# Performance work log

Hardware: AMD Instinct MI355X
Metric: run time of the kernel (lower is better)

Reference implementation:

```python
import jax, jax.numpy as jnp
import numpy as np

N, DIN, DOUT, E, H, C1 = 100000, 1000, 20, 1600000, 8, 8
BN_EPS = 1e-5
NEG_SLOPE = 0.2


def setup_inputs() -> dict:
    key = jax.random.key(0)
    ks = jax.random.split(key, 12)
    s = 0.05
    return {
        "x": jax.random.normal(ks[0], (N, DIN), jnp.float32),
        "edge_index": jax.random.randint(ks[1], (2, E), 0, N, jnp.int32),
        "bn_gamma": jnp.ones((DIN,), jnp.float32),
        "bn_beta": jnp.zeros((DIN,), jnp.float32),
        "W1": jax.random.normal(ks[2], (DIN, H * C1), jnp.float32) * s,
        "a_src1": jax.random.normal(ks[3], (H, C1), jnp.float32) * s,
        "a_dst1": jax.random.normal(ks[4], (H, C1), jnp.float32) * s,
        "b1": jnp.zeros((H * C1,), jnp.float32),
        "W2": jax.random.normal(ks[5], (H * C1, H * DOUT), jnp.float32) * s,
        "a_src2": jax.random.normal(ks[6], (H, DOUT), jnp.float32) * s,
        "a_dst2": jax.random.normal(ks[7], (H, DOUT), jnp.float32) * s,
        "b2": jnp.zeros((DOUT,), jnp.float32),
    }


def _gat(x, src, dst, W, a_src, a_dst, bias, heads, out_ch, concat):
    n = x.shape[0]
    h = (x @ W).reshape(n, heads, out_ch)              # [N,H,C]
    al_s = jnp.sum(h * a_src, axis=-1)                 # [N,H]
    al_d = jnp.sum(h * a_dst, axis=-1)                 # [N,H]
    e = al_s[src] + al_d[dst]                          # [E,H]
    e = jnp.where(e >= 0, e, NEG_SLOPE * e)            # leaky_relu(0.2)
    # segment softmax over incoming edges of each dst node
    m = jax.ops.segment_max(e, dst, num_segments=n)
    m = jnp.where(jnp.isfinite(m), m, 0.0)
    ex = jnp.exp(e - m[dst])
    denom = jax.ops.segment_sum(ex, dst, num_segments=n)
    alpha = ex / (denom[dst] + 1e-16)                  # [E,H]
    msg = h[src] * alpha[:, :, None]                   # [E,H,C]
    out = jax.ops.segment_sum(msg, dst, num_segments=n)  # [N,H,C]
    out = out.reshape(n, heads * out_ch) if concat else out.mean(axis=1)
    return out + bias


def reference(x, edge_index, bn_gamma, bn_beta, W1, a_src1, a_dst1, b1, W2, a_src2, a_dst2, b2):
    # BatchNorm1d (training-mode batch statistics, biased variance)
    mu = x.mean(axis=0)
    var = x.var(axis=0)
    xn = (x - mu) * jax.lax.rsqrt(var + BN_EPS) * bn_gamma + bn_beta
    # add self loops (PyG GATConv default add_self_loops=True)
    loops = jnp.arange(N, dtype=edge_index.dtype)
    src = jnp.concatenate([edge_index[0], loops])
    dst = jnp.concatenate([edge_index[1], loops])
    h = _gat(xn, src, dst, W1, a_src1, a_dst1, b1, H, C1, True)
    h = jax.nn.elu(h)
    out = _gat(h, src, dst, W2, a_src2, a_dst2, b2, H, DOUT, False)
    return jax.nn.log_softmax(out, axis=1)
```

## Files before the change

kernel.cpp:

```cpp
#include <hip/hip_runtime.h>
#include <math.h>

#define N_NODES 100000
#define D_IN    1000
#define D_OUT   20
#define N_HEAD  8
#define C_ONE   8
#define SCAN_CHUNK 512
#define NCH ((N_NODES + SCAN_CHUNK - 1) / SCAN_CHUNK)

#define BM 128
#define BN 64
#define BK 64
#define KPAD 1024
#define KTILES 16
#define G1_BLOCKS ((N_NODES + BM - 1) / BM)
#define BN_BLOCKS 500
#define NPART BN_BLOCKS
#define PREP_BLOCKS 297

static constexpr float kBnEps = 1e-5f;
static constexpr float kSlope = 0.2f;

typedef __attribute__((ext_vector_type(8))) short short8;
typedef __attribute__((ext_vector_type(4))) short sh4;
typedef __attribute__((ext_vector_type(4))) float f32x4;

__device__ __forceinline__ unsigned short f2bf(float f) {
    unsigned u = __float_as_uint(f);
    unsigned r = (u + 0x7fffu + ((u >> 16) & 1u)) >> 16;
    return (unsigned short)r;
}
__device__ __forceinline__ float bf2f(short s) {
    unsigned u = ((unsigned)(unsigned short)s) << 16;
    return __uint_as_float(u);
}

__global__ __launch_bounds__(256) void k_phase1(const float* __restrict__ x,
                                                float* __restrict__ ps,
                                                const int* __restrict__ ei,
                                                int E, int TE,
                                                int* __restrict__ deg) {
    int b = blockIdx.x, tid = threadIdx.x;
    if (b < BN_BLOCKS) {
        int c4 = tid;
        if (c4 >= 250) return;
        int r0 = b * 200;
        float4 s = make_float4(0.f, 0.f, 0.f, 0.f);
        float4 q = make_float4(0.f, 0.f, 0.f, 0.f);
        const char* base = (const char*)x + (size_t)r0 * (D_IN * 4) + (size_t)c4 * 16;
        for (int i = 0; i < 200; i += 8) {
            float4 v[8];
            #pragma unroll
            for (int j = 0; j < 8; ++j)
                v[j] = *(const float4*)(base + (size_t)(i + j) * (D_IN * 4));
            #pragma unroll
            for (int j = 0; j < 8; ++j) {
                s.x += v[j].x; s.y += v[j].y; s.z += v[j].z; s.w += v[j].w;
                q.x += v[j].x * v[j].x; q.y += v[j].y * v[j].y;
                q.z += v[j].z * v[j].z; q.w += v[j].w * v[j].w;
            }
        }
        *(float4*)(ps + (size_t)b * 2000 + c4 * 4) = s;
        *(float4*)(ps + (size_t)b * 2000 + 1000 + c4 * 4) = q;
    } else {
        int eid = (b - BN_BLOCKS) * 256 + tid;
        if (eid >= TE) return;
        int dst = (eid < E) ? ei[E + eid] : (eid - E);
        atomicAdd(&deg[dst], 1);
    }
}

__global__ void k_reduce(const float* __restrict__ ps,
                         float* __restrict__ cs, float* __restrict__ cs2) {
    int cg = blockIdx.x & 3;
    int ch = blockIdx.x >> 2;
    int c = cg * 256 + threadIdx.x;
    if (c >= D_IN) return;
    int b0 = ch * (NPART / 10), b1 = b0 + (NPART / 10);
    float s = 0.f, s2 = 0.f;
    #pragma unroll 5
    for (int b = b0; b < b1; ++b) {
        s  += ps[(size_t)b * 2000 + c];
        s2 += ps[(size_t)b * 2000 + 1000 + c];
    }
    atomicAdd(&cs[c], s);
    atomicAdd(&cs2[c], s2);
}

__global__ void k_phase2(const int* __restrict__ deg, int* __restrict__ csum,
                         const float* __restrict__ W1, const float* __restrict__ W2,
                         const float* __restrict__ cs, const float* __restrict__ cs2,
                         const float* __restrict__ gamma, const float* __restrict__ beta,
                         short* __restrict__ W1t, short* __restrict__ W2t,
                         float* __restrict__ c1) {
    __shared__ int red[4];
    __shared__ float part[4][64];
    int b = blockIdx.x, tid = threadIdx.x;
    if (b < NCH) {
        int i0 = b * SCAN_CHUNK + tid * 2;
        int a = (i0 < N_NODES) ? deg[i0] : 0;
        int bb = (i0 + 1 < N_NODES) ? deg[i0 + 1] : 0;
        int t = a + bb;
        #pragma unroll
        for (int d = 1; d < 64; d <<= 1) t += __shfl_xor(t, d);
        if ((tid & 63) == 0) red[tid >> 6] = t;
        __syncthreads();
        if (tid == 0) csum[b] = red[0] + red[1] + red[2] + red[3];
        return;
    }
    int pb = b - NCH;
    if (pb < 256) {
        int idx = pb * 256 + tid;
        int n = idx >> 10, k = idx & (KPAD - 1);
        float v = 0.f;
        if (k < D_IN) {
            float mu  = cs[k]  * (1.f / N_NODES);
            float var = cs2[k] * (1.f / N_NODES) - mu * mu;
            float sc  = rsqrtf(var + kBnEps) * gamma[k];
            v = W1[k * 64 + n] * sc;
        }
        W1t[idx] = (short)f2bf(v);
    } else if (pb < 296) {
        int idx = (pb - 256) * 256 + tid;
        if (idx < 160 * 64) {
            int n = idx >> 6, k = idx & 63;
            W2t[idx] = (short)f2bf(W2[k * 160 + n]);
        }
    } else {
        int j  = tid & 63;
        int kc = tid >> 6;
        float acc = 0.f;
        for (int k = kc * 250; k < (kc + 1) * 250; ++k) {
            float mu  = cs[k]  * (1.f / N_NODES);
            float var = cs2[k] * (1.f / N_NODES) - mu * mu;
            float sc  = rsqrtf(var + kBnEps) * gamma[k];
            float sh  = beta[k] - mu * sc;
            acc += sh * W1[k * 64 + j];
        }
        part[kc][j] = acc;
        __syncthreads();
        if (kc == 0) c1[j] = part[0][j] + part[1][j] + part[2][j] + part[3][j];
    }
}

__global__ void k_scan_c(const int* __restrict__ deg, const int* __restrict__ csum,
                         int TE, int* __restrict__ row_start, int* __restrict__ cursor) {
    __shared__ int wsum1[4];
    __shared__ int wsum2[4];
    __shared__ int base_sh;
    int c = blockIdx.x, tid = threadIdx.x;
    int lane = tid & 63, w = tid >> 6;

    int pv = (tid < c) ? csum[tid] : 0;
    #pragma unroll
    for (int d = 1; d < 64; d <<= 1) pv += __shfl_xor(pv, d);
    if (lane == 0) wsum1[w] = pv;
    __syncthreads();
    if (tid == 0) base_sh = wsum1[0] + wsum1[1] + wsum1[2] + wsum1[3];

    int i0 = c * SCAN_CHUNK + tid * 2;
    int a = (i0 < N_NODES) ? deg[i0] : 0;
    int b = (i0 + 1 < N_NODES) ? deg[i0 + 1] : 0;
    int t = a + b;
    int incl = t;
    #pragma unroll
    for (int d = 1; d < 64; d <<= 1) {
        int v = __shfl_up(incl, d);
        if (lane >= d) incl += v;
    }
    if (lane == 63) wsum2[w] = incl;
    __syncthreads();
    int wbase = 0;
    for (int k = 0; k < w; ++k) wbase += wsum2[k];
    int ex = base_sh + wbase + incl - t;
    if (i0 < N_NODES)     { row_start[i0] = ex;         cursor[i0] = ex; }
    if (i0 + 1 < N_NODES) { row_start[i0 + 1] = ex + a; cursor[i0 + 1] = ex + a; }
    if (c == 0 && tid == 0) row_start[N_NODES] = TE;
}

__global__ __launch_bounds__(256) void k_phase4(const float* __restrict__ x,
                                                const short* __restrict__ W1t,
                                                const float* __restrict__ c1,
                                                const float* __restrict__ a_src1,
                                                const float* __restrict__ a_dst1,
                                                short* __restrict__ h1b,
                                                float* __restrict__ als,
                                                float* __restrict__ ald,
                                                const int* __restrict__ ei,
                                                int E, int TE,
                                                int* __restrict__ cursor,
                                                int* __restrict__ srcs) {
    __shared__ short lA[BM * BK];
    __shared__ short lB[BN * BK];

    int tid = threadIdx.x;
    if ((int)blockIdx.x >= G1_BLOCKS) {
        int eid = ((int)blockIdx.x - G1_BLOCKS) * 256 + tid;
        if (eid < TE) {
            int src, dst;
            if (eid < E) { src = ei[eid]; dst = ei[E + eid]; }
            else { src = eid - E; dst = src; }
            int pos = atomicAdd(&cursor[dst], 1);
            srcs[pos] = src;
        }
        return;
    }

    int lane = tid & 63;
    int wave = tid >> 6;
    int l15  = lane & 15, kq = lane >> 4;
    int row0 = blockIdx.x * BM;
    int wm0  = wave * 32;

    f32x4 zero4 = {0.f, 0.f, 0.f, 0.f};
    f32x4 acc[2][4];
    #pragma unroll
    for (int m = 0; m < 2; ++m)
        #pragma unroll
        for (int n = 0; n < 4; ++n) acc[m][n] = zero4;

    int ar = tid >> 4;
    int akf4 = tid & 15;

    for (int kt = 0; kt < KTILES; ++kt) {
        int k0 = kt * BK;
        bool kok = (k0 + akf4 * 4) < D_IN;
        #pragma unroll
        for (int p = 0; p < 8; ++p) {
            int r = ar + p * 16;
            int gr = row0 + r;
            float4 v = make_float4(0.f, 0.f, 0.f, 0.f);
            if (gr < N_NODES && kok)
                v = *(const float4*)(x + (size_t)gr * D_IN + k0 + akf4 * 4);
            unsigned lo = f2bf(v.x) | ((unsigned)f2bf(v.y) << 16);
            unsigned hi = f2bf(v.z) | ((unsigned)f2bf(v.w) << 16);
            int off = r * 128 + ((((akf4 >> 1) ^ (r & 7)) << 4) | ((akf4 & 1) << 3));
            *(uint2*)((char*)lA + off) = make_uint2(lo, hi);
        }
        #pragma unroll
        for (int c = tid; c < 512; c += 256) {
            int n = c >> 3, s = c & 7;
            short8 v = *(const short8*)((const char*)W1t + n * (KPAD * 2) + k0 * 2 + (s << 4));
            int off = n * 128 + ((s ^ (n & 7)) << 4);
            *(short8*)((char*)lB + off) = v;
        }
        __syncthreads();
        #pragma unroll
        for (int h = 0; h < 2; ++h) {
            short8 aF[2], bF[4];
            #pragma unroll
            for (int m = 0; m < 2; ++m) {
                int row = wm0 + m * 16 + l15;
                int off = row * 128 + (((((h << 2) + kq)) ^ (row & 7)) << 4);
                aF[m] = *(const short8*)((const char*)lA + off);
            }
            #pragma unroll
            for (int n = 0; n < 4; ++n) {
                int col = n * 16 + l15;
                int off = col * 128 + (((((h << 2) + kq)) ^ (col & 7)) << 4);
                bF[n] = *(const short8*)((const char*)lB + off);
            }
            #pragma unroll
            for (int m = 0; m < 2; ++m)
                #pragma unroll
                for (int n = 0; n < 4; ++n)
                    acc[m][n] = __builtin_amdgcn_mfma_f32_16x16x32_bf16(aF[m], bF[n], acc[m][n], 0, 0, 0);
        }
        __syncthreads();
    }

    float cv[4];
    #pragma unroll
    for (int n = 0; n < 4; ++n) cv[n] = c1[n * 16 + l15];
    #pragma unroll
    for (int m = 0; m < 2; ++m)
        #pragma unroll
        for (int q = 0; q < 4; ++q) {
            int rl = wm0 + m * 16 + (kq << 2) + q;
            #pragma unroll
            for (int n = 0; n < 4; ++n)
                lA[rl * 64 + n * 16 + l15] = (short)f2bf(acc[m][n][q] + cv[n]);
        }
    __syncthreads();
    #pragma unroll
    for (int idx = tid; idx < 1024; idx += 256) {
        int r = idx >> 3, s = idx & 7;
        int gr = row0 + r;
        if (gr < N_NODES)
            *(short8*)((char*)h1b + (size_t)gr * 128 + (s << 4)) =
                *(const short8*)((const char*)lA + r * 128 + (s << 4));
    }
    #pragma unroll
    for (int pair = tid; pair < 1024; pair += 256) {
        int r = pair >> 3, hd = pair & 7;
        int gr = row0 + r;
        if (gr >= N_NODES) continue;
        short8 v = *(const short8*)((const char*)lA + r * 128 + hd * 16);
        float s = 0.f, d = 0.f;
        #pragma unroll
        for (int c = 0; c < 8; ++c) {
            float f = bf2f(v[c]);
            s += f * a_src1[hd * 8 + c];
            d += f * a_dst1[hd * 8 + c];
        }
        als[gr * 8 + hd] = s;
        ald[gr * 8 + hd] = d;
    }
}

__global__ __launch_bounds__(512) void k_fused_l2(const int* __restrict__ row_start,
                                                  const int* __restrict__ srcs,
                                                  const float* __restrict__ als1,
                                                  const float* __restrict__ ald1,
                                                  const short* __restrict__ h1b,
                                                  const float* __restrict__ b1,
                                                  const short* __restrict__ W2t,
                                                  const float* __restrict__ a_src2,
                                                  const float* __restrict__ a_dst2,
                                                  short* __restrict__ h2b,
                                                  float* __restrict__ als2,
                                                  float* __restrict__ ald2) {
    __shared__ __align__(16) char smem[40960];
    short* lA  = (short*)smem;
    short* lB  = (short*)(smem + 16384);
    short* stg = (short*)smem;

    int tid  = threadIdx.x;
    int lane = tid & 63;
    int wave = tid >> 6;
    int l15  = lane & 15, kq = lane >> 4;
    int row0 = blockIdx.x * 128;
    int wm0  = wave * 16;

    for (int idx = tid; idx < 1280; idx += 512) {
        int n = idx >> 3, s = idx & 7;
        short8 v = *(const short8*)((const char*)W2t + n * 128 + (s << 4));
        int off = n * 128 + ((s ^ (n & 7)) << 4);
        *(short8*)((char*)lB + off) = v;
    }

    #pragma unroll
    for (int pp = 0; pp < 2; ++pp) {
        int pair = tid + pp * 512;
        int r = pair >> 3, hd = pair & 7;
        int dst = row0 + r;
        short8 o = {0, 0, 0, 0, 0, 0, 0, 0};
        if (dst < N_NODES) {
            int beg = row_start[dst], end = row_start[dst + 1];
            float ad = ald1[dst * 8 + hd];
            float sum = 0.f;
            float acc[C_ONE] = {};
            for (int e = beg; e < end; ++e) {
                int s = srcs[e];
                float v = als1[s * 8 + hd] + ad;
                v = v >= 0.f ? v : kSlope * v;
                float wgt = __expf(v);
                short8 hv = *(const short8*)((const char*)h1b + (size_t)s * 128 + hd * 16);
                sum += wgt;
                #pragma unroll
                for (int c = 0; c < C_ONE; ++c) acc[c] += wgt * bf2f(hv[c]);
            }
            float inv = 1.f / (sum + 1e-16f);
            #pragma unroll
            for (int c = 0; c < C_ONE; ++c) {
                float v = acc[c] * inv + b1[hd * 8 + c];
                v = v > 0.f ? v : __expf(v) - 1.f;
                o[c] = (short)f2bf(v);
            }
        }
        int off = r * 128 + ((hd ^ (r & 7)) << 4);
        *(short8*)((char*)lA + off) = o;
    }
    __syncthreads();

    f32x4 zero4 = {0.f, 0.f, 0.f, 0.f};
    f32x4 acc2[10];
    #pragma unroll
    for (int n = 0; n < 10; ++n) acc2[n] = zero4;

    #pragma unroll
    for (int hh = 0; hh < 2; ++hh) {
        short8 aF, bF[10];
        {
            int row = wm0 + l15;
            int off = row * 128 + ((((hh << 2) + kq) ^ (row & 7)) << 4);
            aF = *(const short8*)((const char*)lA + off);
        }
        #pragma unroll
        for (int n = 0; n < 10; ++n) {
            int col = n * 16 + l15;
            int off = col * 128 + ((((hh << 2) + kq) ^ (col & 7)) << 4);
            bF[n] = *(const short8*)((const char*)lB + off);
        }
        #pragma unroll
        for (int n = 0; n < 10; ++n)
            acc2[n] = __builtin_amdgcn_mfma_f32_16x16x32_bf16(aF, bF[n], acc2[n], 0, 0, 0);
    }
    __syncthreads();

    #pragma unroll
    for (int q = 0; q < 4; ++q) {
        int rl = wm0 + (kq << 2) + q;
        #pragma unroll
        for (int n = 0; n < 10; ++n)
            stg[rl * 160 + n * 16 + l15] = (short)f2bf(acc2[n][q]);
    }
    __syncthreads();

    for (int pair = tid; pair < 1024; pair += 512) {
        int r = pair >> 3, hd = pair & 7;
        int dst = row0 + r;
        if (dst >= N_NODES) continue;
        const char* hp = (const char*)stg + r * 320 + hd * 40;
        float s = 0.f, d = 0.f;
        #pragma unroll
        for (int p = 0; p < 5; ++p) {
            sh4 v = *(const sh4*)(hp + p * 8);
            #pragma unroll
            for (int j = 0; j < 4; ++j) {
                float f = bf2f(v[j]);
                s += f * a_src2[hd * 20 + p * 4 + j];
                d += f * a_dst2[hd * 20 + p * 4 + j];
            }
        }
        als2[dst * 8 + hd] = s;
        ald2[dst * 8 + hd] = d;
    }
    for (int idx = tid; idx < 2560; idx += 512) {
        int r = idx / 20, c8 = idx % 20;
        int gr = row0 + r;
        if (gr < N_NODES)
            *(short8*)((char*)h2b + (size_t)gr * 320 + (c8 << 4)) =
                *(const short8*)((const char*)stg + r * 320 + (c8 << 4));
    }
}

__global__ __launch_bounds__(256) void k_gather2(const int* __restrict__ row_start,
                                                 const int* __restrict__ srcs,
                                                 const float* __restrict__ als,
                                                 const float* __restrict__ ald,
                                                 const short* __restrict__ h2,
                                                 const float* __restrict__ b2,
                                                 float* __restrict__ out) {
    int idx = blockIdx.x * blockDim.x + threadIdx.x;
    if (idx >= N_NODES * 16) return;
    int dst  = idx >> 4;
    int sub  = idx & 15;
    int hd   = sub >> 1;
    int half = sub & 1;
    int beg0 = row_start[dst], end0 = row_start[dst + 1];
    int mid  = beg0 + ((end0 - beg0 + 1) >> 1);
    int beg  = half ? mid : beg0;
    int end  = half ? end0 : mid;
    float ad = ald[dst * 8 + hd];
    float sum = 0.f;
    float acc[D_OUT] = {};
    for (int e = beg; e < end; ++e) {
        int s = srcs[e];
        float v = als[s * 8 + hd] + ad;
        v = v >= 0.f ? v : kSlope * v;
        float wgt = __expf(v);
        const char* hp = (const char*)h2 + (size_t)s * 320 + hd * 40;
        sum += wgt;
        #pragma unroll
        for (int p = 0; p < 5; ++p) {
            sh4 t = *(const sh4*)(hp + p * 8);
            #pragma unroll
            for (int j = 0; j < 4; ++j) acc[p * 4 + j] += wgt * bf2f(t[j]);
        }
    }
    sum += __shfl_xor(sum, 1);
    float inv = 1.f / (sum + 1e-16f);
    #pragma unroll
    for (int c = 0; c < D_OUT; ++c) {
        float v = acc[c];
        v += __shfl_xor(v, 1);
        v *= inv;
        v += __shfl_xor(v, 2);
        v += __shfl_xor(v, 4);
        v += __shfl_xor(v, 8);
        acc[c] = v;
    }
    if (sub == 0) {
        float vals[D_OUT];
        float mx = -1e30f;
        #pragma unroll
        for (int c = 0; c < D_OUT; ++c) {
            vals[c] = 0.125f * acc[c] + b2[c];
            mx = fmaxf(mx, vals[c]);
        }
        float s = 0.f;
        #pragma unroll
        for (int c = 0; c < D_OUT; ++c) s += __expf(vals[c] - mx);
        float lse = mx + __logf(s);
        float* op = out + (size_t)dst * D_OUT;
        #pragma unroll
        for (int c = 0; c < D_OUT; ++c) op[c] = vals[c] - lse;
    }
}

extern "C" void kernel_launch(void* const* d_in, const int* in_sizes, int n_in,
                              void* d_out, int out_size, void* d_ws, size_t ws_size,
                              hipStream_t stream) {
    const float* x      = (const float*)d_in[0];
    const int*   ei     = (const int*)d_in[1];
    const float* gamma  = (const float*)d_in[2];
    const float* beta   = (const float*)d_in[3];
    const float* W1     = (const float*)d_in[4];
    const float* a_src1 = (const float*)d_in[5];
    const float* a_dst1 = (const float*)d_in[6];
    const float* b1     = (const float*)d_in[7];
    const float* W2     = (const float*)d_in[8];
    const float* a_src2 = (const float*)d_in[9];
    const float* a_dst2 = (const float*)d_in[10];
    const float* b2     = (const float*)d_in[11];
    float* out = (float*)d_out;
    (void)n_in; (void)out_size; (void)ws_size;

    const int E  = in_sizes[1] / 2;
    const int TE = E + N_NODES;

    char* wsb = (char*)d_ws;
    size_t off = 0;
    auto alloc = [&](size_t bytes) -> void* {
        void* p = wsb + off;
        off += (bytes + 255) & ~(size_t)255;
        return p;
    };
    float* cs    = (float*)alloc(D_IN * sizeof(float));
    float* cs2   = (float*)alloc(D_IN * sizeof(float));
    float* ps    = (float*)alloc((size_t)NPART * 2000 * sizeof(float));
    short* W1t   = (short*)alloc((size_t)64 * KPAD * sizeof(short));
    short* W2t   = (short*)alloc((size_t)160 * 64 * sizeof(short));
    float* c1    = (float*)alloc(64 * sizeof(float));
    short* h1b   = (short*)alloc((size_t)N_NODES * 64 * sizeof(short));
    short* h2b   = (short*)alloc((size_t)N_NODES * 160 * sizeof(short));
    float* als   = (float*)alloc((size_t)N_NODES * N_HEAD * sizeof(float));
    float* ald   = (float*)alloc((size_t)N_NODES * N_HEAD * sizeof(float));
    float* als2  = (float*)alloc((size_t)N_NODES * N_HEAD * sizeof(float));
    float* ald2  = (float*)alloc((size_t)N_NODES * N_HEAD * sizeof(float));
    int*   deg   = (int*)alloc((size_t)N_NODES * sizeof(int));
    int*   rs    = (int*)alloc((size_t)(N_NODES + 1) * sizeof(int));
    int*   cur   = (int*)alloc((size_t)N_NODES * sizeof(int));
    int*   csum  = (int*)alloc((size_t)NCH * sizeof(int));
    int*   srcs  = (int*)alloc((size_t)TE * sizeof(int));

    int egrid = (TE + 255) / 256;

    hipMemsetAsync(deg, 0, (size_t)N_NODES * sizeof(int), stream);
    hipMemsetAsync(cs, 0, 8192, stream);

    k_phase1<<<BN_BLOCKS + egrid, 256, 0, stream>>>(x, ps, ei, E, TE, deg);

    k_reduce<<<40, 256, 0, stream>>>(ps, cs, cs2);

    k_phase2<<<NCH + PREP_BLOCKS, 256, 0, stream>>>(deg, csum, W1, W2, cs, cs2,
                                                     gamma, beta, W1t, W2t, c1);

    k_scan_c<<<NCH, 256, 0, stream>>>(deg, csum, TE, rs, cur);

    k_phase4<<<G1_BLOCKS + egrid, 256, 0, stream>>>(x, W1t, c1, a_src1, a_dst1,
                                                     h1b, als, ald, ei, E, TE, cur, srcs);

    k_fused_l2<<<(N_NODES + 127) / 128, 512, 0, stream>>>(rs, srcs, als, ald, h1b, b1,
                                                           W2t, a_src2, a_dst2,
                                                           h2b, als2, ald2);

    k_gather2<<<(N_NODES * 16 + 255) / 256, 256, 0, stream>>>(rs, srcs, als2, ald2,
                                                               h2b, b2, out);
}
```

Measured before the change: 460.8 us.

## Reassociate layer-2 GAT: aggregate 64-wide features before applying W2

Layer 2 no longer projects every node to 160 features. Instead it stores the 64-wide ELU output. The attention logits come from precomputed folded vectors, W2·a_src2 and W2·a_dst2. The gather kernel builds per-head weighted sums of the 64-wide source features, sharing each head's weight across 8 lanes with shuffles. It then applies W2 once per destination node. This cuts per-edge gather bytes and removes the MFMA projection and the large h2 write. The cost is more per-edge FMAs (64 per lane), more registers, and a per-node matvec that reads W2t from global memory.

```diff
diff --git a/kernel.cpp b/kernel.cpp
--- a/kernel.cpp
+++ b/kernel.cpp
@@ -17,7 +17,7 @@
 #define G1_BLOCKS ((N_NODES + BM - 1) / BM)
 #define BN_BLOCKS 500
 #define NPART BN_BLOCKS
-#define PREP_BLOCKS 297
+#define PREP_BLOCKS 298
 
 static constexpr float kBnEps = 1e-5f;
 static constexpr float kSlope = 0.2f;
@@ -92,8 +92,10 @@
                          const float* __restrict__ W1, const float* __restrict__ W2,
                          const float* __restrict__ cs, const float* __restrict__ cs2,
                          const float* __restrict__ gamma, const float* __restrict__ beta,
+                         const float* __restrict__ a_src2, const float* __restrict__ a_dst2,
                          short* __restrict__ W1t, short* __restrict__ W2t,
-                         float* __restrict__ c1) {
+                         float* __restrict__ c1,
+                         float* __restrict__ wt_s, float* __restrict__ wt_d) {
     __shared__ int red[4];
     __shared__ float part[4][64];
     int b = blockIdx.x, tid = threadIdx.x;
@@ -127,7 +129,7 @@
             int n = idx >> 6, k = idx & 63;
             W2t[idx] = (short)f2bf(W2[k * 160 + n]);
         }
-    } else {
+    } else if (pb == 296) {
         int j  = tid & 63;
         int kc = tid >> 6;
         float acc = 0.f;
@@ -141,6 +143,21 @@
         part[kc][j] = acc;
         __syncthreads();
         if (kc == 0) c1[j] = part[0][j] + part[1][j] + part[2][j] + part[3][j];
+    } else {
+        #pragma unroll
+        for (int it = 0; it < 2; ++it) {
+            int idx = it * 256 + tid;
+            int h = idx >> 6, k = idx & 63;
+            float ss = 0.f, dd = 0.f;
+            #pragma unroll
+            for (int c = 0; c < 20; ++c) {
+                float w = W2[k * 160 + h * 20 + c];
+                ss += w * a_src2[h * 20 + c];
+                dd += w * a_dst2[h * 20 + c];
+            }
+            wt_s[h * 64 + k] = ss;
+            wt_d[h * 64 + k] = dd;
+        }
     }
 }
 
@@ -315,30 +332,19 @@
                                                   const float* __restrict__ ald1,
                                                   const short* __restrict__ h1b,
                                                   const float* __restrict__ b1,
-                                                  const short* __restrict__ W2t,
-                                                  const float* __restrict__ a_src2,
-                                                  const float* __restrict__ a_dst2,
-                                                  short* __restrict__ h2b,
+                                                  const float* __restrict__ wt_s,
+                                                  const float* __restrict__ wt_d,
+                                                  short* __restrict__ out1b,
                                                   float* __restrict__ als2,
                                                   float* __restrict__ ald2) {
-    __shared__ __align__(16) char smem[40960];
-    short* lA  = (short*)smem;
-    short* lB  = (short*)(smem + 16384);
-    short* stg = (short*)smem;
+    __shared__ short lA[128 * 64];
+    __shared__ float lWs[512];
+    __shared__ float lWd[512];
 
     int tid  = threadIdx.x;
-    int lane = tid & 63;
-    int wave = tid >> 6;
-    int l15  = lane & 15, kq = lane >> 4;
     int row0 = blockIdx.x * 128;
-    int wm0  = wave * 16;
-
-    for (int idx = tid; idx < 1280; idx += 512) {
-        int n = idx >> 3, s = idx & 7;
-        short8 v = *(const short8*)((const char*)W2t + n * 128 + (s << 4));
-        int off = n * 128 + ((s ^ (n & 7)) << 4);
-        *(short8*)((char*)lB + off) = v;
-    }
+
+    if (tid < 512) { lWs[tid] = wt_s[tid]; lWd[tid] = wt_d[tid]; }
 
     #pragma unroll
     for (int pp = 0; pp < 2; ++pp) {
@@ -374,65 +380,35 @@
     }
     __syncthreads();
 
-    f32x4 zero4 = {0.f, 0.f, 0.f, 0.f};
-    f32x4 acc2[10];
-    #pragma unroll
-    for (int n = 0; n < 10; ++n) acc2[n] = zero4;
-
-    #pragma unroll
-    for (int hh = 0; hh < 2; ++hh) {
-        short8 aF, bF[10];
-        {
-            int row = wm0 + l15;
-            int off = row * 128 + ((((hh << 2) + kq) ^ (row & 7)) << 4);
-            aF = *(const short8*)((const char*)lA + off);
-        }
-        #pragma unroll
-        for (int n = 0; n < 10; ++n) {
-            int col = n * 16 + l15;
-            int off = col * 128 + ((((hh << 2) + kq) ^ (col & 7)) << 4);
-            bF[n] = *(const short8*)((const char*)lB + off);
-        }
-        #pragma unroll
-        for (int n = 0; n < 10; ++n)
-            acc2[n] = __builtin_amdgcn_mfma_f32_16x16x32_bf16(aF, bF[n], acc2[n], 0, 0, 0);
-    }
-    __syncthreads();
-
-    #pragma unroll
-    for (int q = 0; q < 4; ++q) {
-        int rl = wm0 + (kq << 2) + q;
-        #pragma unroll
-        for (int n = 0; n < 10; ++n)
-            stg[rl * 160 + n * 16 + l15] = (short)f2bf(acc2[n][q]);
-    }
-    __syncthreads();
-
-    for (int pair = tid; pair < 1024; pair += 512) {
+    #pragma unroll
+    for (int pp = 0; pp < 2; ++pp) {
+        int idx = tid + pp * 512;
+        int r = idx >> 3, s = idx & 7;
+        int gr = row0 + r;
+        if (gr < N_NODES)
+            *(short8*)((char*)out1b + (size_t)gr * 128 + (s << 4)) =
+                *(const short8*)((const char*)lA + r * 128 + ((s ^ (r & 7)) << 4));
+    }
+
+    #pragma unroll
+    for (int pp = 0; pp < 2; ++pp) {
+        int pair = tid + pp * 512;
         int r = pair >> 3, hd = pair & 7;
         int dst = row0 + r;
         if (dst >= N_NODES) continue;
-        const char* hp = (const char*)stg + r * 320 + hd * 40;
         float s = 0.f, d = 0.f;
         #pragma unroll
-        for (int p = 0; p < 5; ++p) {
-            sh4 v = *(const sh4*)(hp + p * 8);
-            #pragma unroll
-            for (int j = 0; j < 4; ++j) {
-                float f = bf2f(v[j]);
-                s += f * a_src2[hd * 20 + p * 4 + j];
-                d += f * a_dst2[hd * 20 + p * 4 + j];
+        for (int ch = 0; ch < 8; ++ch) {
+            short8 v = *(const short8*)((const char*)lA + r * 128 + ((ch ^ (r & 7)) << 4));
+            #pragma unroll
+            for (int c = 0; c < 8; ++c) {
+                float f = bf2f(v[c]);
+                s += f * lWs[hd * 64 + ch * 8 + c];
+                d += f * lWd[hd * 64 + ch * 8 + c];
             }
         }
         als2[dst * 8 + hd] = s;
         ald2[dst * 8 + hd] = d;
-    }
-    for (int idx = tid; idx < 2560; idx += 512) {
-        int r = idx / 20, c8 = idx % 20;
-        int gr = row0 + r;
-        if (gr < N_NODES)
-            *(short8*)((char*)h2b + (size_t)gr * 320 + (c8 << 4)) =
-                *(const short8*)((const char*)stg + r * 320 + (c8 << 4));
     }
 }
 
@@ -440,60 +416,91 @@
                                                  const int* __restrict__ srcs,
                                                  const float* __restrict__ als,
                                                  const float* __restrict__ ald,
-                                                 const short* __restrict__ h2,
+                                                 const short* __restrict__ out1b,
+                                                 const short* __restrict__ W2t,
                                                  const float* __restrict__ b2,
                                                  float* __restrict__ out) {
-    int idx = blockIdx.x * blockDim.x + threadIdx.x;
-    if (idx >= N_NODES * 16) return;
-    int dst  = idx >> 4;
-    int sub  = idx & 15;
-    int hd   = sub >> 1;
-    int half = sub & 1;
-    int beg0 = row_start[dst], end0 = row_start[dst + 1];
-    int mid  = beg0 + ((end0 - beg0 + 1) >> 1);
-    int beg  = half ? mid : beg0;
-    int end  = half ? end0 : mid;
-    float ad = ald[dst * 8 + hd];
-    float sum = 0.f;
-    float acc[D_OUT] = {};
+    int tid = threadIdx.x;
+    int g = tid >> 3, j = tid & 7;
+    int dst = blockIdx.x * 32 + g;
+    if (dst >= N_NODES) return;
+
+    int beg = row_start[dst], end = row_start[dst + 1];
+    float adj = ald[dst * 8 + j];
+    float Agg[8][8] = {};
+    float mysum = 0.f;
+
     for (int e = beg; e < end; ++e) {
         int s = srcs[e];
-        float v = als[s * 8 + hd] + ad;
+        float v = als[s * 8 + j] + adj;
         v = v >= 0.f ? v : kSlope * v;
-        float wgt = __expf(v);
-        const char* hp = (const char*)h2 + (size_t)s * 320 + hd * 40;
-        sum += wgt;
-        #pragma unroll
-        for (int p = 0; p < 5; ++p) {
-            sh4 t = *(const sh4*)(hp + p * 8);
-            #pragma unroll
-            for (int j = 0; j < 4; ++j) acc[p * 4 + j] += wgt * bf2f(t[j]);
-        }
-    }
-    sum += __shfl_xor(sum, 1);
-    float inv = 1.f / (sum + 1e-16f);
+        float w = __expf(v);
+        mysum += w;
+        float a0 = w;
+        float a1 = __shfl_xor(a0, 1);
+        float a2 = __shfl_xor(a0, 2);
+        float a3 = __shfl_xor(a1, 2);
+        float a4 = __shfl_xor(a0, 4);
+        float a5 = __shfl_xor(a1, 4);
+        float a6 = __shfl_xor(a2, 4);
+        float a7 = __shfl_xor(a3, 4);
+        short8 hv = *(const short8*)((const char*)out1b + (size_t)s * 128 + j * 16);
+        float f[8];
+        #pragma unroll
+        for (int c = 0; c < 8; ++c) f[c] = bf2f(hv[c]);
+        #pragma unroll
+        for (int c = 0; c < 8; ++c) {
+            Agg[0][c] += a0 * f[c];
+            Agg[1][c] += a1 * f[c];
+            Agg[2][c] += a2 * f[c];
+            Agg[3][c] += a3 * f[c];
+            Agg[4][c] += a4 * f[c];
+            Agg[5][c] += a5 * f[c];
+            Agg[6][c] += a6 * f[c];
+            Agg[7][c] += a7 * f[c];
+        }
+    }
+
+    float s0 = mysum;
+    float s1 = __shfl_xor(s0, 1);
+    float s2 = __shfl_xor(s0, 2);
+    float s3 = __shfl_xor(s1, 2);
+    float s4 = __shfl_xor(s0, 4);
+    float s5 = __shfl_xor(s1, 4);
+    float s6 = __shfl_xor(s2, 4);
+    float s7 = __shfl_xor(s3, 4);
+    float iS[8];
+    iS[0] = 1.f / (s0 + 1e-16f); iS[1] = 1.f / (s1 + 1e-16f);
+    iS[2] = 1.f / (s2 + 1e-16f); iS[3] = 1.f / (s3 + 1e-16f);
+    iS[4] = 1.f / (s4 + 1e-16f); iS[5] = 1.f / (s5 + 1e-16f);
+    iS[6] = 1.f / (s6 + 1e-16f); iS[7] = 1.f / (s7 + 1e-16f);
+
+    float vals[D_OUT];
     #pragma unroll
     for (int c = 0; c < D_OUT; ++c) {
-        float v = acc[c];
-        v += __shfl_xor(v, 1);
-        v *= inv;
-        v += __shfl_xor(v, 2);
-        v += __shfl_xor(v, 4);
-        v += __shfl_xor(v, 8);
-        acc[c] = v;
-    }
-    if (sub == 0) {
-        float vals[D_OUT];
+        float pv = 0.f;
+        #pragma unroll
+        for (int m = 0; m < 8; ++m) {
+            int h = j ^ m;
+            short8 wv = *(const short8*)((const char*)W2t + (((h * 20 + c) << 6) + (j << 3)) * 2);
+            float dot = 0.f;
+            #pragma unroll
+            for (int k = 0; k < 8; ++k) dot += Agg[m][k] * bf2f(wv[k]);
+            pv += iS[m] * dot;
+        }
+        pv += __shfl_xor(pv, 1);
+        pv += __shfl_xor(pv, 2);
+        pv += __shfl_xor(pv, 4);
+        vals[c] = 0.125f * pv + b2[c];
+    }
+    if (j == 0) {
         float mx = -1e30f;
         #pragma unroll
-        for (int c = 0; c < D_OUT; ++c) {
-            vals[c] = 0.125f * acc[c] + b2[c];
-            mx = fmaxf(mx, vals[c]);
-        }
-        float s = 0.f;
-        #pragma unroll
-        for (int c = 0; c < D_OUT; ++c) s += __expf(vals[c] - mx);
-        float lse = mx + __logf(s);
+        for (int c = 0; c < D_OUT; ++c) mx = fmaxf(mx, vals[c]);
+        float ssum = 0.f;
+        #pragma unroll
+        for (int c = 0; c < D_OUT; ++c) ssum += __expf(vals[c] - mx);
+        float lse = mx + __logf(ssum);
         float* op = out + (size_t)dst * D_OUT;
         #pragma unroll
         for (int c = 0; c < D_OUT; ++c) op[c] = vals[c] - lse;
@@ -534,8 +541,10 @@
     short* W1t   = (short*)alloc((size_t)64 * KPAD * sizeof(short));
     short* W2t   = (short*)alloc((size_t)160 * 64 * sizeof(short));
     float* c1    = (float*)alloc(64 * sizeof(float));
+    float* wts   = (float*)alloc(512 * sizeof(float));
+    float* wtd   = (float*)alloc(512 * sizeof(float));
     short* h1b   = (short*)alloc((size_t)N_NODES * 64 * sizeof(short));
-    short* h2b   = (short*)alloc((size_t)N_NODES * 160 * sizeof(short));
+    short* out1b = (short*)alloc((size_t)N_NODES * 64 * sizeof(short));
     float* als   = (float*)alloc((size_t)N_NODES * N_HEAD * sizeof(float));
     float* ald   = (float*)alloc((size_t)N_NODES * N_HEAD * sizeof(float));
     float* als2  = (float*)alloc((size_t)N_NODES * N_HEAD * sizeof(float));
@@ -556,7 +565,8 @@
     k_reduce<<<40, 256, 0, stream>>>(ps, cs, cs2);
 
     k_phase2<<<NCH + PREP_BLOCKS, 256, 0, stream>>>(deg, csum, W1, W2, cs, cs2,
-                                                     gamma, beta, W1t, W2t, c1);
+                                                     gamma, beta, a_src2, a_dst2,
+                                                     W1t, W2t, c1, wts, wtd);
 
     k_scan_c<<<NCH, 256, 0, stream>>>(deg, csum, TE, rs, cur);
 
@@ -564,9 +574,8 @@
                                                      h1b, als, ald, ei, E, TE, cur, srcs);
 
     k_fused_l2<<<(N_NODES + 127) / 128, 512, 0, stream>>>(rs, srcs, als, ald, h1b, b1,
-                                                           W2t, a_src2, a_dst2,
-                                                           h2b, als2, ald2);
-
-    k_gather2<<<(N_NODES * 16 + 255) / 256, 256, 0, stream>>>(rs, srcs, als2, ald2,
-                                                               h2b, b2, out);
-}
+                                                           wts, wtd, out1b, als2, ald2);
+
+    k_gather2<<<(N_NODES + 31) / 32, 256, 0, stream>>>(rs, srcs, als2, ald2,
+                                                        out1b, W2t, b2, out);
+}
```

New measurement: 611.8 us (median of 3 runs). +32.8%, slower.
